# Optimization experiments

Hardware: AMD Instinct MI355X
Metric: run time of the kernel (lower is better)

Reference implementation:

```python
import jax, jax.numpy as jnp
import numpy as np
from math import sqrt

MIN_WINDOW, MAX_WINDOW = 1.0, 10000.0


def rope_consecutive(x):
    # x: [B, S, H, D]; TE 'consecutive' rotary: pairs are adjacent (even, odd) lanes.
    d = x.shape[-1]
    half = d // 2
    fraction = 2.0 * jnp.arange(half, dtype=jnp.float32) / d
    time_scales = MIN_WINDOW * (MAX_WINDOW / MIN_WINDOW) ** fraction          # [D/2]
    time_scales = jnp.repeat(time_scales, 2)                                   # [D]
    positions = jnp.arange(x.shape[1], dtype=jnp.float32)                      # [S]
    sinusoid = positions[None, :, None, None] / time_scales                    # [1,S,1,D]
    sin, cos = jnp.sin(sinusoid), jnp.cos(sinusoid)
    idx = jnp.arange(d)
    odd = (idx % 2) == 1                                                       # [D]
    # even lanes take left neighbor (roll -1), odd lanes take right neighbor (roll +1)
    x_shifted = jnp.where(odd, jnp.roll(x, 1, axis=-1), jnp.roll(x, -1, axis=-1))
    sign = jnp.where(odd, 1.0, -1.0)
    return (x * cos + x_shifted * sin * sign).astype(x.dtype)


def setup_inputs() -> dict:
    key = jax.random.key(0)
    k1, k2, k3 = jax.random.split(key, 3)
    B, S, M, H, D = 4, 2048, 2048, 16, 128
    x = jax.random.normal(k1, (B, S, M), dtype=jnp.float32)
    Wqkv = jax.random.normal(k2, (M, 3, H, D), dtype=jnp.float32) / sqrt(M)
    Wo = jax.random.normal(k3, (H * D, M), dtype=jnp.float32) / sqrt(H * D)
    return {"x": x, "Wqkv": Wqkv, "Wo": Wo}


def reference(x, Wqkv, Wo):
    # x: [B,S,M]; Wqkv: [M,3,H,D]; Wo: [H*D,M]
    B, S, M = x.shape
    H, D = Wqkv.shape[2], Wqkv.shape[3]
    qkv = jnp.einsum('bsm,mthd->bsthd', x, Wqkv)  # packed BS3HD projection
    q, k, v = qkv[:, :, 0], qkv[:, :, 1], qkv[:, :, 2]  # each [B,S,H,D]
    q = rope_consecutive(q)
    k = rope_consecutive(k)
    scale = 1.0 / sqrt(D)
    scores = jnp.einsum('bqhd,bkhd->bhqk', q, k) * scale  # [B,H,S,S]
    causal = jnp.tril(jnp.ones((S, S), dtype=bool))
    scores = jnp.where(causal[None, None], scores, jnp.finfo(scores.dtype).min)
    probs = jax.nn.softmax(scores, axis=-1)
    ctx = jnp.einsum('bhqk,bkhd->bqhd', probs, v)  # [B,S,H,D]
    out = jnp.einsum('bqhd,xm->bqm', ctx, jnp.zeros((0, 0))) if False else ctx.reshape(B, S, H * D) @ Wo
    return out
```

## Files before the change

kernel.cpp:

```cpp
#include <hip/hip_runtime.h>
#include <hip/hip_bf16.h>

#define B_ 4
#define S_ 2048
#define M_ 2048
#define H_ 16
#define D_ 128
#define ROWS (B_*S_)
#define CQKV (3*H_*D_)

typedef __bf16 bf16x8 __attribute__((ext_vector_type(8)));
typedef float f32x4 __attribute__((ext_vector_type(4)));
typedef unsigned short u16x8 __attribute__((ext_vector_type(8)));
typedef unsigned short u16x4 __attribute__((ext_vector_type(4)));

__device__ __forceinline__ unsigned short f2bf(float x) {
    unsigned u = __builtin_bit_cast(unsigned, x);
    u += 0x7fffu + ((u >> 16) & 1u);
    return (unsigned short)(u >> 16);
}
__device__ __forceinline__ float bf2f(unsigned short u) {
    return __builtin_bit_cast(float, (unsigned)u << 16);
}

__device__ __forceinline__ void gld_lds16(const unsigned short* g, unsigned short* l) {
    __builtin_amdgcn_global_load_lds(
        (__attribute__((address_space(1))) void*)g,
        (__attribute__((address_space(3))) void*)l,
        16, 0, 0);
}


__global__ __launch_bounds__(256) void cvt_bf16(const float* __restrict__ in,
                                                unsigned short* __restrict__ out) {
    int idx = (blockIdx.x * 256 + threadIdx.x) * 4;
    float4 v = *(const float4*)&in[idx];
    u16x4 o = { f2bf(v.x), f2bf(v.y), f2bf(v.z), f2bf(v.w) };
    *(u16x4*)&out[idx] = o;
}

__global__ __launch_bounds__(256) void cvt_transpose(const float* __restrict__ in,
                                                     unsigned short* __restrict__ out,
                                                     int R, int C) {
    __shared__ unsigned short tile[32][33];
    int c0 = blockIdx.x * 32, r0 = blockIdx.y * 32;
    int tx = threadIdx.x, ty = threadIdx.y;
#pragma unroll
    for (int i = 0; i < 4; ++i)
        tile[ty + i * 8][tx] = f2bf(in[(size_t)(r0 + ty + i * 8) * C + c0 + tx]);
    __syncthreads();
#pragma unroll
    for (int i = 0; i < 4; ++i)
        out[(size_t)(c0 + ty + i * 8) * R + r0 + tx] = tile[tx][ty + i * 8];
}

__global__ __launch_bounds__(256) void vtrans(const unsigned short* __restrict__ in,
                                              unsigned short* __restrict__ out) {
    __shared__ unsigned short tile[32][33];
    int bh = blockIdx.z;
    int d0 = blockIdx.x * 32, s0 = blockIdx.y * 32;
    const unsigned short* ib = in + (size_t)bh * S_ * D_;
    unsigned short* ob = out + (size_t)bh * S_ * D_;
    int tx = threadIdx.x, ty = threadIdx.y;
#pragma unroll
    for (int i = 0; i < 4; ++i)
        tile[ty + i * 8][tx] = ib[(size_t)(s0 + ty + i * 8) * D_ + d0 + tx];
    __syncthreads();
#pragma unroll
    for (int i = 0; i < 4; ++i)
        ob[(size_t)(d0 + ty + i * 8) * S_ + s0 + tx] = tile[tx][ty + i * 8];
}


#define BM2 256
#define BN2 256
#define BK2 64
#define NT2 (M_/BK2)

#define STAGE(p_, u_, mat_, h_) do {                                                     \
        const unsigned short* _s = (mat_) ? Bg : Ag;                                     \
        const size_t _r = (size_t)((((mat_) ? c0 : r0) + (h_) * 128) + w * 8 + srow) * M_ \
                          + (u_) * BK2 + scol;                                           \
        unsigned short* _l = &lds[(p_) * 32768 + (mat_) * 16384 + (h_) * 8192 + w * 512]; \
        gld_lds16(&_s[_r], _l);                                                          \
        gld_lds16(&_s[_r + (size_t)64 * M_], _l + 4096);                                 \
    } while (0)

#define BAR() asm volatile("s_barrier" ::: "memory")

#define GEMM_MAIN_LOOP()                                                                  \
    const int srow = lane >> 3;                                                           \
    const int scol = ((lane & 7) ^ srow) * 8;                                             \
    const int axor = lcol & 7;                                                            \
    const int k0off = (lq ^ axor) * 8;                                                    \
    const int k1off = ((4 | lq) ^ axor) * 8;                                              \
    const int arow = wr * 8192 + lcol * 64;                                               \
    const int brow = 16384 + (wc >> 1) * 8192 + ((wc & 1) * 64 + lcol) * 64;              \
    f32x4 acc[8][4];                                                                      \
    _Pragma("unroll") for (int i = 0; i < 8; ++i)                                         \
        _Pragma("unroll") for (int j = 0; j < 4; ++j) acc[i][j] = (f32x4){0.f,0.f,0.f,0.f};\
    STAGE(0, 0, 0, 0); STAGE(0, 0, 0, 1); STAGE(0, 0, 1, 0); STAGE(0, 0, 1, 1);           \
    STAGE(1, 1, 1, 0); STAGE(1, 1, 1, 1);                                                 \
    asm volatile("s_waitcnt vmcnt(4)" ::: "memory");                                      \
    BAR();                                                                                \
    bf16x8 a[4][2], b[4][2];                                                              \
    for (int t = 0; t < NT2; ++t) {                                                       \
        const int bo = (t & 1) * 32768;                                                   \
        const int pn = (t + 1) & 1;                                                       \
        const int u1 = (t + 1 < NT2) ? (t + 1) : (NT2 - 1);                               \
        const int u2 = (t + 2 < NT2) ? (t + 2) : (NT2 - 1);                               \
        _Pragma("unroll") for (int i = 0; i < 4; ++i) {                                   \
            a[i][0] = *(const bf16x8*)&lds[bo + arow + i * 1024 + k0off];                  \
            a[i][1] = *(const bf16x8*)&lds[bo + arow + i * 1024 + k1off];                  \
        }                                                                                 \
        _Pragma("unroll") for (int j = 0; j < 2; ++j) {                                   \
            b[j][0] = *(const bf16x8*)&lds[bo + brow + j * 1024 + k0off];                  \
            b[j][1] = *(const bf16x8*)&lds[bo + brow + j * 1024 + k1off];                  \
        }                                                                                 \
        STAGE(pn, u1, 0, 0);                                                              \
        BAR();                                                                            \
        __builtin_amdgcn_s_setprio(1);                                                    \
        _Pragma("unroll") for (int i = 0; i < 4; ++i)                                     \
            _Pragma("unroll") for (int j = 0; j < 2; ++j) {                               \
                acc[i][j] = __builtin_amdgcn_mfma_f32_16x16x32_bf16(a[i][0], b[j][0], acc[i][j], 0, 0, 0); \
                acc[i][j] = __builtin_amdgcn_mfma_f32_16x16x32_bf16(a[i][1], b[j][1], acc[i][j], 0, 0, 0); \
            }                                                                             \
        __builtin_amdgcn_s_setprio(0);                                                    \
        BAR();                                                                            \
        _Pragma("unroll") for (int j = 2; j < 4; ++j) {                                   \
            b[j][0] = *(const bf16x8*)&lds[bo + brow + j * 1024 + k0off];                  \
            b[j][1] = *(const bf16x8*)&lds[bo + brow + j * 1024 + k1off];                  \
        }                                                                                 \
        STAGE(pn, u1, 0, 1);                                                              \
        BAR();                                                                            \
        __builtin_amdgcn_s_setprio(1);                                                    \
        _Pragma("unroll") for (int i = 0; i < 4; ++i)                                     \
            _Pragma("unroll") for (int j = 2; j < 4; ++j) {                               \
                acc[i][j] = __builtin_amdgcn_mfma_f32_16x16x32_bf16(a[i][0], b[j][0], acc[i][j], 0, 0, 0); \
                acc[i][j] = __builtin_amdgcn_mfma_f32_16x16x32_bf16(a[i][1], b[j][1], acc[i][j], 0, 0, 0); \
            }                                                                             \
        __builtin_amdgcn_s_setprio(0);                                                    \
        BAR();                                                                            \
        _Pragma("unroll") for (int i = 0; i < 4; ++i) {                                   \
            a[i][0] = *(const bf16x8*)&lds[bo + arow + (i + 4) * 1024 + k0off];            \
            a[i][1] = *(const bf16x8*)&lds[bo + arow + (i + 4) * 1024 + k1off];            \
        }                                                                                 \
        STAGE(t & 1, u2, 1, 0);                                                           \
        BAR();                                                                            \
        __builtin_amdgcn_s_setprio(1);                                                    \
        _Pragma("unroll") for (int i = 0; i < 4; ++i)                                     \
            _Pragma("unroll") for (int j = 2; j < 4; ++j) {                               \
                acc[i + 4][j] = __builtin_amdgcn_mfma_f32_16x16x32_bf16(a[i][0], b[j][0], acc[i + 4][j], 0, 0, 0); \
                acc[i + 4][j] = __builtin_amdgcn_mfma_f32_16x16x32_bf16(a[i][1], b[j][1], acc[i + 4][j], 0, 0, 0); \
            }                                                                             \
        __builtin_amdgcn_s_setprio(0);                                                    \
        BAR();                                                                            \
        STAGE(t & 1, u2, 1, 1);                                                           \
        BAR();                                                                            \
        __builtin_amdgcn_s_setprio(1);                                                    \
        _Pragma("unroll") for (int i = 0; i < 4; ++i)                                     \
            _Pragma("unroll") for (int j = 0; j < 2; ++j) {                               \
                acc[i + 4][j] = __builtin_amdgcn_mfma_f32_16x16x32_bf16(a[i][0], b[j][0], acc[i + 4][j], 0, 0, 0); \
                acc[i + 4][j] = __builtin_amdgcn_mfma_f32_16x16x32_bf16(a[i][1], b[j][1], acc[i + 4][j], 0, 0, 0); \
            }                                                                             \
        __builtin_amdgcn_s_setprio(0);                                                    \
        asm volatile("s_waitcnt vmcnt(4)" ::: "memory");                                  \
        BAR();                                                                            \
    }


__global__ __launch_bounds__(512, 2) void gemm_qkv_rope(
    const unsigned short* __restrict__ xb,
    const unsigned short* __restrict__ wT,
    unsigned short* __restrict__ qg,
    unsigned short* __restrict__ kg,
    unsigned short* __restrict__ vg) {
    __shared__ unsigned short lds[65536];

    const int tid = threadIdx.x;
    const int lane = tid & 63;
    const int w = tid >> 6;
    const int wr = w >> 2;
    const int wc = w & 3;
    const int lcol = lane & 15;
    const int lq = lane >> 4;

    const int lin = (int)(blockIdx.y * gridDim.x + blockIdx.x);
    const int swz = (lin & 7) * 96 + (lin >> 3);
    const int r0 = (swz / 24) * BM2;
    const int c0 = (swz % 24) * BN2;

    const unsigned short* Ag = xb;
    const unsigned short* Bg = wT;

    GEMM_MAIN_LOOP()

    const int colbase = c0 + wc * 64;
    const int tix = colbase >> 11;
    const int hh = (colbase & 2047) >> 7;
    unsigned short* dst = (tix == 0) ? qg : (tix == 1) ? kg : vg;
    if (tix < 2) {
#pragma unroll
        for (int j = 0; j < 4; ++j) {
            const int d = (wc & 1) * 64 + j * 16 + lcol;
            float inv_ts = exp2f(-(float)(d >> 1) * (13.28771237954945f / 64.0f));
            float sw, cw;
            __sincosf(inv_ts, &sw, &cw);
#pragma unroll
            for (int i = 0; i < 8; ++i) {
                int row0 = r0 + wr * 128 + i * 16 + lq * 4;
                int bb = row0 >> 11, s0 = row0 & 2047;
                float sn, cs;
                __sincosf((float)s0 * inv_ts, &sn, &cs);
                size_t base = (size_t)((bb * H_ + hh) * S_ + s0) * D_ + d;
#pragma unroll
                for (int r = 0; r < 4; ++r) {
                    float val = acc[i][j][r];
                    float pr = __shfl_xor(val, 1);
                    float v2 = (d & 1) ? (val * cs + pr * sn) : (val * cs - pr * sn);
                    dst[base + (size_t)r * D_] = f2bf(v2);
                    float ns = sn * cw + cs * sw;
                    float nc = cs * cw - sn * sw;
                    sn = ns; cs = nc;
                }
            }
        }
    } else {
#pragma unroll
        for (int j = 0; j < 4; ++j) {
            const int d = (wc & 1) * 64 + j * 16 + lcol;
#pragma unroll
            for (int i = 0; i < 8; ++i) {
                int row0 = r0 + wr * 128 + i * 16 + lq * 4;
                int bb = row0 >> 11, s0 = row0 & 2047;
                size_t base = (size_t)((bb * H_ + hh) * S_ + s0) * D_ + d;
#pragma unroll
                for (int r = 0; r < 4; ++r)
                    dst[base + (size_t)r * D_] = f2bf(acc[i][j][r]);
            }
        }
    }
}


__global__ __launch_bounds__(512, 2) void gemm_out(
    const unsigned short* __restrict__ ctx,
    const unsigned short* __restrict__ woT,
    float* __restrict__ out) {
    __shared__ unsigned short lds[65536];

    const int tid = threadIdx.x;
    const int lane = tid & 63;
    const int w = tid >> 6;
    const int wr = w >> 2;
    const int wc = w & 3;
    const int lcol = lane & 15;
    const int lq = lane >> 4;

    const int lin = (int)(blockIdx.y * gridDim.x + blockIdx.x);
    const int swz = (lin & 7) * 32 + (lin >> 3);
    const int r0 = (swz >> 3) * BM2;
    const int c0 = (swz & 7) * BN2;

    const unsigned short* Ag = ctx;
    const unsigned short* Bg = woT;

    GEMM_MAIN_LOOP()

#pragma unroll
    for (int i = 0; i < 8; ++i) {
#pragma unroll
        for (int r = 0; r < 4; ++r) {
            int row = r0 + wr * 128 + i * 16 + lq * 4 + r;
#pragma unroll
            for (int j = 0; j < 4; ++j) {
                int col = c0 + wc * 64 + j * 16 + lcol;
                out[(size_t)row * M_ + col] = acc[i][j][r];
            }
        }
    }
}

#undef STAGE
#undef BAR


__global__ __launch_bounds__(512, 4) void attn(
    const unsigned short* __restrict__ qg,
    const unsigned short* __restrict__ kg,
    const unsigned short* __restrict__ vt,
    unsigned short* __restrict__ ctx) {
    __shared__ unsigned short Ks[64 * 136];
    __shared__ unsigned short VTs[128 * 72];
    __shared__ unsigned short Ps[128 * 72];

    const int tid = threadIdx.x, lane = tid & 63, wave = tid >> 6;

    const int lin = (int)(blockIdx.y * gridDim.x + blockIdx.x);
    const int idx = lin >> 3;
    const int bh = ((lin & 7) << 3) + (idx >> 4);
    const int q0 = (15 - (idx & 15)) * 128;
    const int q0b = q0 + wave * 16;
    const unsigned short* qb = qg + (size_t)bh * S_ * D_;
    const unsigned short* kb = kg + (size_t)bh * S_ * D_;
    const unsigned short* vtb = vt + (size_t)bh * S_ * D_;

    const int lcol = lane & 15;
    const int lq = lane >> 4;

    const float scale = 0.08838834764831845f;
    bf16x8 qf[4];
#pragma unroll
    for (int kk = 0; kk < 4; ++kk) {
        u16x8 raw = *(const u16x8*)&qb[(size_t)(q0b + lcol) * D_ + kk * 32 + lq * 8];
        u16x8 sc8;
#pragma unroll
        for (int j = 0; j < 8; ++j) sc8[j] = f2bf(bf2f(raw[j]) * scale);
        qf[kk] = __builtin_bit_cast(bf16x8, sc8);
    }

    f32x4 o[8];
#pragma unroll
    for (int ot = 0; ot < 8; ++ot) o[ot] = (f32x4){0.f, 0.f, 0.f, 0.f};
    float lsum[4] = {0.f, 0.f, 0.f, 0.f};

    const int kv_last = q0 + 64;

    u16x8 kpre[2], vpre[2];
#pragma unroll
    for (int j = 0; j < 2; ++j) {
        int c = tid + j * 512;
        kpre[j] = *(const u16x8*)&kb[(size_t)(c >> 4) * D_ + (c & 15) * 8];
        vpre[j] = *(const u16x8*)&vtb[(size_t)(c >> 3) * S_ + (c & 7) * 8];
    }

    for (int kv0 = 0; kv0 <= kv_last; kv0 += 64) {
        __syncthreads();
#pragma unroll
        for (int j = 0; j < 2; ++j) {
            int c = tid + j * 512;
            *(u16x8*)&Ks[(c >> 4) * 136 + (c & 15) * 8] = kpre[j];
            *(u16x8*)&VTs[(c >> 3) * 72 + (c & 7) * 8] = vpre[j];
        }
        __syncthreads();
        if (kv0 + 64 <= kv_last) {
#pragma unroll
            for (int j = 0; j < 2; ++j) {
                int c = tid + j * 512;
                kpre[j] = *(const u16x8*)&kb[(size_t)(kv0 + 64 + (c >> 4)) * D_ + (c & 15) * 8];
                vpre[j] = *(const u16x8*)&vtb[(size_t)(c >> 3) * S_ + kv0 + 64 + (c & 7) * 8];
            }
        }

        if (kv0 <= q0b) {
            f32x4 sc[4];
            __builtin_amdgcn_s_setprio(1);
#pragma unroll
            for (int nt = 0; nt < 4; ++nt) {
                f32x4 a = (f32x4){0.f, 0.f, 0.f, 0.f};
#pragma unroll
                for (int kk = 0; kk < 4; ++kk) {
                    bf16x8 kf = *(const bf16x8*)&Ks[(nt * 16 + lcol) * 136 + kk * 32 + lq * 8];
                    a = __builtin_amdgcn_mfma_f32_16x16x32_bf16(qf[kk], kf, a, 0, 0, 0);
                }
                sc[nt] = a;
            }
            __builtin_amdgcn_s_setprio(0);

            if (kv0 + 63 > q0b) {
#pragma unroll
                for (int nt = 0; nt < 4; ++nt)
#pragma unroll
                    for (int r = 0; r < 4; ++r) {
                        int skv = kv0 + nt * 16 + lcol;
                        int sq = q0b + lq * 4 + r;
                        float p = (skv > sq) ? 0.f : __expf(sc[nt][r]);
                        sc[nt][r] = p;
                        lsum[r] += p;
                    }
            } else {
#pragma unroll
                for (int nt = 0; nt < 4; ++nt)
#pragma unroll
                    for (int r = 0; r < 4; ++r) {
                        float p = __expf(sc[nt][r]);
                        sc[nt][r] = p;
                        lsum[r] += p;
                    }
            }

#pragma unroll
            for (int nt = 0; nt < 4; ++nt)
#pragma unroll
                for (int r = 0; r < 4; ++r)
                    Ps[(wave * 16 + lq * 4 + r) * 72 + nt * 16 + lcol] = f2bf(sc[nt][r]);

            __builtin_amdgcn_s_setprio(1);
#pragma unroll
            for (int kk = 0; kk < 2; ++kk) {
                bf16x8 pf = *(const bf16x8*)&Ps[(wave * 16 + lcol) * 72 + kk * 32 + lq * 8];
#pragma unroll
                for (int ot = 0; ot < 8; ++ot) {
                    bf16x8 vf = *(const bf16x8*)&VTs[(ot * 16 + lcol) * 72 + kk * 32 + lq * 8];
                    o[ot] = __builtin_amdgcn_mfma_f32_16x16x32_bf16(pf, vf, o[ot], 0, 0, 0);
                }
            }
            __builtin_amdgcn_s_setprio(0);
        }
    }

#pragma unroll
    for (int r = 0; r < 4; ++r) {
#pragma unroll
        for (int off = 1; off < 16; off <<= 1) lsum[r] += __shfl_xor(lsum[r], off);
    }

    const int b = bh >> 4, h = bh & 15;
#pragma unroll
    for (int r = 0; r < 4; ++r) {
        float invl = 1.0f / lsum[r];
        int s = q0b + lq * 4 + r;
#pragma unroll
        for (int ot = 0; ot < 8; ++ot) {
            int d = ot * 16 + lcol;
            ctx[(size_t)(b * S_ + s) * (H_ * D_) + h * D_ + d] = f2bf(o[ot][r] * invl);
        }
    }
}


extern "C" void kernel_launch(void* const* d_in, const int* in_sizes, int n_in,
                              void* d_out, int out_size, void* d_ws, size_t ws_size,
                              hipStream_t stream) {
    const float* x = (const float*)d_in[0];
    const float* Wqkv = (const float*)d_in[1];
    const float* Wo = (const float*)d_in[2];
    float* out = (float*)d_out;

    unsigned short* xb = (unsigned short*)d_ws;
    unsigned short* wT = xb + (size_t)ROWS * M_;
    unsigned short* woT = wT + (size_t)CQKV * M_;
    unsigned short* qg = woT + (size_t)M_ * M_;
    unsigned short* kg = qg + (size_t)B_ * H_ * S_ * D_;
    unsigned short* vg = kg + (size_t)B_ * H_ * S_ * D_;
    unsigned short* vtw = vg + (size_t)B_ * H_ * S_ * D_;
    unsigned short* ctxp = vtw + (size_t)B_ * H_ * S_ * D_;

    cvt_bf16<<<(ROWS * M_) / 1024, 256, 0, stream>>>(x, xb);
    cvt_transpose<<<dim3(CQKV / 32, M_ / 32), dim3(32, 8), 0, stream>>>(Wqkv, wT, M_, CQKV);
    cvt_transpose<<<dim3(M_ / 32, M_ / 32), dim3(32, 8), 0, stream>>>(Wo, woT, M_, M_);

    gemm_qkv_rope<<<dim3(CQKV / BN2, ROWS / BM2), 512, 0, stream>>>(xb, wT, qg, kg, vg);
    vtrans<<<dim3(D_ / 32, S_ / 32, B_ * H_), dim3(32, 8), 0, stream>>>(vg, vtw);
    attn<<<dim3(S_ / 128, B_ * H_), 512, 0, stream>>>(qg, kg, vtw, ctxp);
    gemm_out<<<dim3(M_ / BN2, ROWS / BM2), 512, 0, stream>>>(ctxp, woT, out);
}
```

Baseline: 582.3 us.

## Stage QKV epilogue through LDS for coalesced stores; widen attention waves to 32 rows

The QKV GEMM epilogue now applies RoPE, writes the bf16 results into a swizzled LDS tile, then issues coalesced 16-byte stores to the head-major Q/K/V buffers. This replaces the scattered 2-byte global stores. The attention kernel moves to 256-thread blocks in which each wave handles 32 query rows. Every K/V fragment read from LDS then feeds two MFMAs, which cuts LDS traffic per FLOP but raises register pressure and lowers wave count per block. The epilogue assumes the GEMM's LDS buffer is large enough and can be reused once the main loop has finished.

```diff
diff --git a/kernel.cpp b/kernel.cpp
--- a/kernel.cpp
+++ b/kernel.cpp
@@ -195,50 +195,62 @@
 
     GEMM_MAIN_LOOP()
 
-    const int colbase = c0 + wc * 64;
-    const int tix = colbase >> 11;
-    const int hh = (colbase & 2047) >> 7;
-    unsigned short* dst = (tix == 0) ? qg : (tix == 1) ? kg : vg;
-    if (tix < 2) {
-#pragma unroll
-        for (int j = 0; j < 4; ++j) {
-            const int d = (wc & 1) * 64 + j * 16 + lcol;
-            float inv_ts = exp2f(-(float)(d >> 1) * (13.28771237954945f / 64.0f));
-            float sw, cw;
+    asm volatile("s_waitcnt vmcnt(0)" ::: "memory");
+    __syncthreads();
+
+    const int tix = c0 >> 11;
+    const bool do_rope = (tix < 2);
+#pragma unroll
+    for (int j = 0; j < 4; ++j) {
+        const int lcolT = wc * 64 + j * 16 + lcol;
+        const int d = lcolT & 127;
+        float inv_ts = 0.f, sw = 0.f, cw = 1.f;
+        if (do_rope) {
+            inv_ts = exp2f(-(float)(d >> 1) * (13.28771237954945f / 64.0f));
             __sincosf(inv_ts, &sw, &cw);
-#pragma unroll
-            for (int i = 0; i < 8; ++i) {
-                int row0 = r0 + wr * 128 + i * 16 + lq * 4;
-                int bb = row0 >> 11, s0 = row0 & 2047;
-                float sn, cs;
+        }
+#pragma unroll
+        for (int i = 0; i < 8; ++i) {
+            const int rbase = wr * 128 + i * 16 + lq * 4;
+            float sn = 0.f, cs = 1.f;
+            if (do_rope) {
+                int s0 = (r0 + rbase) & 2047;
                 __sincosf((float)s0 * inv_ts, &sn, &cs);
-                size_t base = (size_t)((bb * H_ + hh) * S_ + s0) * D_ + d;
-#pragma unroll
-                for (int r = 0; r < 4; ++r) {
-                    float val = acc[i][j][r];
-                    float pr = __shfl_xor(val, 1);
-                    float v2 = (d & 1) ? (val * cs + pr * sn) : (val * cs - pr * sn);
-                    dst[base + (size_t)r * D_] = f2bf(v2);
+            }
+#pragma unroll
+            for (int r = 0; r < 4; ++r) {
+                const int rowT = rbase + r;
+                float val = acc[i][j][r];
+                float pr = __shfl_xor(val, 1);
+                float v2 = val;
+                if (do_rope) {
+                    v2 = (d & 1) ? (val * cs + pr * sn) : (val * cs - pr * sn);
                     float ns = sn * cw + cs * sw;
                     float nc = cs * cw - sn * sw;
                     sn = ns; cs = nc;
                 }
-            }
-        }
-    } else {
-#pragma unroll
-        for (int j = 0; j < 4; ++j) {
-            const int d = (wc & 1) * 64 + j * 16 + lcol;
-#pragma unroll
-            for (int i = 0; i < 8; ++i) {
-                int row0 = r0 + wr * 128 + i * 16 + lq * 4;
-                int bb = row0 >> 11, s0 = row0 & 2047;
-                size_t base = (size_t)((bb * H_ + hh) * S_ + s0) * D_ + d;
-#pragma unroll
-                for (int r = 0; r < 4; ++r)
-                    dst[base + (size_t)r * D_] = f2bf(acc[i][j][r]);
-            }
-        }
+                const int ch = lcolT >> 3;
+                const int cph = (ch & ~7) | ((ch ^ rowT) & 7);
+                lds[rowT * 256 + cph * 8 + (lcolT & 7)] = f2bf(v2);
+            }
+        }
+    }
+    __syncthreads();
+
+    const int hh = (c0 & 2047) >> 7;
+    unsigned short* dst = (tix == 0) ? qg : (tix == 1) ? kg : vg;
+    const int li = tid & 15;
+    const int g = tid >> 4;
+#pragma unroll
+    for (int gi = 0; gi < 16; ++gi) {
+        const int rh = g + gi * 32;
+        const int row = rh >> 1, half = rh & 1;
+        const int clog = half * 16 + li;
+        const int cph = (clog & ~7) | ((clog ^ row) & 7);
+        u16x8 v = *(const u16x8*)&lds[row * 256 + cph * 8];
+        const int gr = r0 + row;
+        const int s = gr & 2047, bb = gr >> 11;
+        *(u16x8*)&dst[(size_t)((bb * H_ + hh + half) * S_ + s) * D_ + li * 8] = v;
     }
 }
 
@@ -285,7 +297,7 @@
 #undef BAR
 
 
-__global__ __launch_bounds__(512, 4) void attn(
+__global__ __launch_bounds__(256, 2) void attn(
     const unsigned short* __restrict__ qg,
     const unsigned short* __restrict__ kg,
     const unsigned short* __restrict__ vt,
@@ -300,7 +312,7 @@
     const int idx = lin >> 3;
     const int bh = ((lin & 7) << 3) + (idx >> 4);
     const int q0 = (15 - (idx & 15)) * 128;
-    const int q0b = q0 + wave * 16;
+    const int q0w = q0 + wave * 32;
     const unsigned short* qb = qg + (size_t)bh * S_ * D_;
     const unsigned short* kb = kg + (size_t)bh * S_ * D_;
     const unsigned short* vtb = vt + (size_t)bh * S_ * D_;
@@ -309,27 +321,31 @@
     const int lq = lane >> 4;
 
     const float scale = 0.08838834764831845f;
-    bf16x8 qf[4];
-#pragma unroll
-    for (int kk = 0; kk < 4; ++kk) {
-        u16x8 raw = *(const u16x8*)&qb[(size_t)(q0b + lcol) * D_ + kk * 32 + lq * 8];
-        u16x8 sc8;
-#pragma unroll
-        for (int j = 0; j < 8; ++j) sc8[j] = f2bf(bf2f(raw[j]) * scale);
-        qf[kk] = __builtin_bit_cast(bf16x8, sc8);
-    }
-
-    f32x4 o[8];
-#pragma unroll
-    for (int ot = 0; ot < 8; ++ot) o[ot] = (f32x4){0.f, 0.f, 0.f, 0.f};
-    float lsum[4] = {0.f, 0.f, 0.f, 0.f};
+    bf16x8 qf[2][4];
+#pragma unroll
+    for (int f = 0; f < 2; ++f)
+#pragma unroll
+        for (int kk = 0; kk < 4; ++kk) {
+            u16x8 raw = *(const u16x8*)&qb[(size_t)(q0w + f * 16 + lcol) * D_ + kk * 32 + lq * 8];
+            u16x8 sc8;
+#pragma unroll
+            for (int j = 0; j < 8; ++j) sc8[j] = f2bf(bf2f(raw[j]) * scale);
+            qf[f][kk] = __builtin_bit_cast(bf16x8, sc8);
+        }
+
+    f32x4 o[2][8];
+#pragma unroll
+    for (int f = 0; f < 2; ++f)
+#pragma unroll
+        for (int ot = 0; ot < 8; ++ot) o[f][ot] = (f32x4){0.f, 0.f, 0.f, 0.f};
+    float lsum[2][4] = {{0.f, 0.f, 0.f, 0.f}, {0.f, 0.f, 0.f, 0.f}};
 
     const int kv_last = q0 + 64;
 
-    u16x8 kpre[2], vpre[2];
-#pragma unroll
-    for (int j = 0; j < 2; ++j) {
-        int c = tid + j * 512;
+    u16x8 kpre[4], vpre[4];
+#pragma unroll
+    for (int j = 0; j < 4; ++j) {
+        int c = tid + j * 256;
         kpre[j] = *(const u16x8*)&kb[(size_t)(c >> 4) * D_ + (c & 15) * 8];
         vpre[j] = *(const u16x8*)&vtb[(size_t)(c >> 3) * S_ + (c & 7) * 8];
     }
@@ -337,72 +353,78 @@
     for (int kv0 = 0; kv0 <= kv_last; kv0 += 64) {
         __syncthreads();
 #pragma unroll
-        for (int j = 0; j < 2; ++j) {
-            int c = tid + j * 512;
+        for (int j = 0; j < 4; ++j) {
+            int c = tid + j * 256;
             *(u16x8*)&Ks[(c >> 4) * 136 + (c & 15) * 8] = kpre[j];
             *(u16x8*)&VTs[(c >> 3) * 72 + (c & 7) * 8] = vpre[j];
         }
         __syncthreads();
         if (kv0 + 64 <= kv_last) {
 #pragma unroll
-            for (int j = 0; j < 2; ++j) {
-                int c = tid + j * 512;
+            for (int j = 0; j < 4; ++j) {
+                int c = tid + j * 256;
                 kpre[j] = *(const u16x8*)&kb[(size_t)(kv0 + 64 + (c >> 4)) * D_ + (c & 15) * 8];
                 vpre[j] = *(const u16x8*)&vtb[(size_t)(c >> 3) * S_ + kv0 + 64 + (c & 7) * 8];
             }
         }
 
-        if (kv0 <= q0b) {
-            f32x4 sc[4];
+        if (kv0 <= q0w + 31) {
+            f32x4 sc[2][4];
             __builtin_amdgcn_s_setprio(1);
 #pragma unroll
             for (int nt = 0; nt < 4; ++nt) {
-                f32x4 a = (f32x4){0.f, 0.f, 0.f, 0.f};
+                f32x4 a0 = (f32x4){0.f, 0.f, 0.f, 0.f};
+                f32x4 a1 = (f32x4){0.f, 0.f, 0.f, 0.f};
 #pragma unroll
                 for (int kk = 0; kk < 4; ++kk) {
                     bf16x8 kf = *(const bf16x8*)&Ks[(nt * 16 + lcol) * 136 + kk * 32 + lq * 8];
-                    a = __builtin_amdgcn_mfma_f32_16x16x32_bf16(qf[kk], kf, a, 0, 0, 0);
+                    a0 = __builtin_amdgcn_mfma_f32_16x16x32_bf16(qf[0][kk], kf, a0, 0, 0, 0);
+                    a1 = __builtin_amdgcn_mfma_f32_16x16x32_bf16(qf[1][kk], kf, a1, 0, 0, 0);
                 }
-                sc[nt] = a;
+                sc[0][nt] = a0; sc[1][nt] = a1;
             }
             __builtin_amdgcn_s_setprio(0);
 
-            if (kv0 + 63 > q0b) {
+#pragma unroll
+            for (int f = 0; f < 2; ++f) {
+                if (kv0 + 63 > q0w + f * 16) {
+#pragma unroll
+                    for (int nt = 0; nt < 4; ++nt)
+#pragma unroll
+                        for (int r = 0; r < 4; ++r) {
+                            int skv = kv0 + nt * 16 + lcol;
+                            int sq = q0w + f * 16 + lq * 4 + r;
+                            float p = (skv > sq) ? 0.f : __expf(sc[f][nt][r]);
+                            sc[f][nt][r] = p;
+                            lsum[f][r] += p;
+                        }
+                } else {
+#pragma unroll
+                    for (int nt = 0; nt < 4; ++nt)
+#pragma unroll
+                        for (int r = 0; r < 4; ++r) {
+                            float p = __expf(sc[f][nt][r]);
+                            sc[f][nt][r] = p;
+                            lsum[f][r] += p;
+                        }
+                }
 #pragma unroll
                 for (int nt = 0; nt < 4; ++nt)
 #pragma unroll
-                    for (int r = 0; r < 4; ++r) {
-                        int skv = kv0 + nt * 16 + lcol;
-                        int sq = q0b + lq * 4 + r;
-                        float p = (skv > sq) ? 0.f : __expf(sc[nt][r]);
-                        sc[nt][r] = p;
-                        lsum[r] += p;
-                    }
-            } else {
-#pragma unroll
-                for (int nt = 0; nt < 4; ++nt)
-#pragma unroll
-                    for (int r = 0; r < 4; ++r) {
-                        float p = __expf(sc[nt][r]);
-                        sc[nt][r] = p;
-                        lsum[r] += p;
-                    }
-            }
-
-#pragma unroll
-            for (int nt = 0; nt < 4; ++nt)
-#pragma unroll
-                for (int r = 0; r < 4; ++r)
-                    Ps[(wave * 16 + lq * 4 + r) * 72 + nt * 16 + lcol] = f2bf(sc[nt][r]);
+                    for (int r = 0; r < 4; ++r)
+                        Ps[(wave * 32 + f * 16 + lq * 4 + r) * 72 + nt * 16 + lcol] = f2bf(sc[f][nt][r]);
+            }
 
             __builtin_amdgcn_s_setprio(1);
 #pragma unroll
             for (int kk = 0; kk < 2; ++kk) {
-                bf16x8 pf = *(const bf16x8*)&Ps[(wave * 16 + lcol) * 72 + kk * 32 + lq * 8];
+                bf16x8 pf0 = *(const bf16x8*)&Ps[(wave * 32 + lcol) * 72 + kk * 32 + lq * 8];
+                bf16x8 pf1 = *(const bf16x8*)&Ps[(wave * 32 + 16 + lcol) * 72 + kk * 32 + lq * 8];
 #pragma unroll
                 for (int ot = 0; ot < 8; ++ot) {
                     bf16x8 vf = *(const bf16x8*)&VTs[(ot * 16 + lcol) * 72 + kk * 32 + lq * 8];
-                    o[ot] = __builtin_amdgcn_mfma_f32_16x16x32_bf16(pf, vf, o[ot], 0, 0, 0);
+                    o[0][ot] = __builtin_amdgcn_mfma_f32_16x16x32_bf16(pf0, vf, o[0][ot], 0, 0, 0);
+                    o[1][ot] = __builtin_amdgcn_mfma_f32_16x16x32_bf16(pf1, vf, o[1][ot], 0, 0, 0);
                 }
             }
             __builtin_amdgcn_s_setprio(0);
@@ -410,22 +432,26 @@
     }
 
 #pragma unroll
-    for (int r = 0; r < 4; ++r) {
-#pragma unroll
-        for (int off = 1; off < 16; off <<= 1) lsum[r] += __shfl_xor(lsum[r], off);
-    }
+    for (int f = 0; f < 2; ++f)
+#pragma unroll
+        for (int r = 0; r < 4; ++r) {
+#pragma unroll
+            for (int off = 1; off < 16; off <<= 1) lsum[f][r] += __shfl_xor(lsum[f][r], off);
+        }
 
     const int b = bh >> 4, h = bh & 15;
 #pragma unroll
-    for (int r = 0; r < 4; ++r) {
-        float invl = 1.0f / lsum[r];
-        int s = q0b + lq * 4 + r;
-#pragma unroll
-        for (int ot = 0; ot < 8; ++ot) {
-            int d = ot * 16 + lcol;
-            ctx[(size_t)(b * S_ + s) * (H_ * D_) + h * D_ + d] = f2bf(o[ot][r] * invl);
-        }
-    }
+    for (int f = 0; f < 2; ++f)
+#pragma unroll
+        for (int r = 0; r < 4; ++r) {
+            float invl = 1.0f / lsum[f][r];
+            int s = q0w + f * 16 + lq * 4 + r;
+#pragma unroll
+            for (int ot = 0; ot < 8; ++ot) {
+                int d = ot * 16 + lcol;
+                ctx[(size_t)(b * S_ + s) * (H_ * D_) + h * D_ + d] = f2bf(o[f][ot][r] * invl);
+            }
+        }
 }
 
 
@@ -452,6 +478,6 @@
 
     gemm_qkv_rope<<<dim3(CQKV / BN2, ROWS / BM2), 512, 0, stream>>>(xb, wT, qg, kg, vg);
     vtrans<<<dim3(D_ / 32, S_ / 32, B_ * H_), dim3(32, 8), 0, stream>>>(vg, vtw);
-    attn<<<dim3(S_ / 128, B_ * H_), 512, 0, stream>>>(qg, kg, vtw, ctxp);
+    attn<<<dim3(S_ / 128, B_ * H_), 256, 0, stream>>>(qg, kg, vtw, ctxp);
     gemm_out<<<dim3(M_ / BN2, ROWS / BM2), 512, 0, stream>>>(ctxp, woT, out);
 }
```

Result: no change. 579.4 us (-0.5%).
